# Optimization experiments

Hardware: AMD Instinct MI355X
Metric: run time of the kernel (lower is better)

Reference implementation:

```python
import jax, jax.numpy as jnp
import numpy as np

N = 50000      # nodes
E = 800000     # edges
D_IN = 512
D_OUT = 512
EDGE_DIM = 3


def setup_inputs() -> dict:
    key = jax.random.key(0)
    k = jax.random.split(key, 6)
    x = jax.random.normal(k[0], (N, D_IN), dtype=jnp.float32)
    edge_index = jax.random.randint(k[1], (2, E), 0, N, dtype=jnp.int64)
    edge_attr = jax.random.normal(k[2], (E, EDGE_DIM), dtype=jnp.float32)
    # xavier-uniform-ish init for linear weights
    lim1 = (6.0 / (D_IN + D_OUT)) ** 0.5
    lin_w = jax.random.uniform(k[3], (D_OUT, D_IN), minval=-lim1, maxval=lim1, dtype=jnp.float32)
    lin_b = jnp.zeros((D_OUT,), dtype=jnp.float32)
    lim2 = (6.0 / (EDGE_DIM + 1)) ** 0.5
    conf_w = jax.random.uniform(k[4], (1, EDGE_DIM), minval=-lim2, maxval=lim2, dtype=jnp.float32)
    conf_b = jnp.zeros((1,), dtype=jnp.float32)
    return {"x": x, "edge_index": edge_index, "edge_attr": edge_attr,
            "lin_w": lin_w, "lin_b": lin_b, "conf_w": conf_w, "conf_b": conf_b}


def reference(x, edge_index, edge_attr, lin_w, lin_b, conf_w, conf_b):
    row, col = edge_index[0], edge_index[1]
    # edge confidence weight: sigmoid(conf_lin(edge_attr)) -> [E]
    edge_weight = jax.nn.sigmoid(edge_attr @ conf_w.T + conf_b)[:, 0]
    # degree of source nodes (count of row occurrences), inverse sqrt with inf/nan -> 0
    deg = jnp.zeros((x.shape[0],), dtype=x.dtype).at[row].add(1.0)
    deg_safe = jnp.where(deg > 0, deg, 1.0)
    deg_inv_sqrt = jnp.where(deg > 0, jax.lax.rsqrt(deg_safe), 0.0)
    norm = deg_inv_sqrt[row] * deg_inv_sqrt[col] * edge_weight  # [E]
    norm = jnp.where(jnp.isnan(norm), 0.0, norm)
    # gather-scale-scatter: out[col] += x[row] * norm
    out = jnp.zeros_like(x).at[col].add(x[row] * norm[:, None])
    return out @ lin_w.T + lin_b
```

## Files before the change

kernel.cpp:

```cpp
#include <hip/hip_runtime.h>

#define NDIM 512
#define CAP  64

typedef __bf16 bf16x8 __attribute__((ext_vector_type(8)));
typedef float  f32x4  __attribute__((ext_vector_type(4)));

__device__ inline ushort f2bf(float f) {
    uint b = __float_as_uint(f);
    return (ushort)((b + 0x7fffu + ((b >> 16) & 1u)) >> 16);
}
__device__ inline float bflo(uint u) { return __uint_as_float(u << 16); }
__device__ inline float bfhi(uint u) { return __uint_as_float(u & 0xffff0000u); }
__device__ inline uint packbf(float lo, float hi) {
    return ((uint)f2bf(hi) << 16) | (uint)f2bf(lo);
}

__device__ inline void gload16(const ushort* g, ushort* l) {
    __builtin_amdgcn_global_load_lds(
        (const __attribute__((address_space(1))) uint*)g,
        (__attribute__((address_space(3))) uint*)l, 16, 0, 0);
}

__global__ __launch_bounds__(256) void prep_kernel(
        const float* __restrict__ x,  ushort* __restrict__ xh,
        const float* __restrict__ w,  ushort* __restrict__ wh,
        const int* __restrict__ ei, int* __restrict__ deg_row,
        int nx4, int nw4, int E, int gX, int gW) {
    int b = blockIdx.x;
    if (b < gX) {
        int i = b * 256 + threadIdx.x;
        if (i < nx4) {
            float4 v = ((const float4*)x)[i];
            ushort4 o;
            o.x = f2bf(v.x); o.y = f2bf(v.y); o.z = f2bf(v.z); o.w = f2bf(v.w);
            ((ushort4*)xh)[i] = o;
        }
    } else if (b < gX + gW) {
        int i = (b - gX) * 256 + threadIdx.x;
        if (i < nw4) {
            float4 v = ((const float4*)w)[i];
            ushort4 o;
            o.x = f2bf(v.x); o.y = f2bf(v.y); o.z = f2bf(v.z); o.w = f2bf(v.w);
            ((ushort4*)wh)[i] = o;
        }
    } else {
        int e = (b - gX - gW) * 256 + threadIdx.x;
        if (e < E) atomicAdd(&deg_row[ei[e]], 1);
    }
}

__global__ __launch_bounds__(256) void fill_kernel(
        const int* __restrict__ ei, const float* __restrict__ ea,
        const int* __restrict__ deg,
        const float* __restrict__ conf_w, const float* __restrict__ conf_b,
        int* __restrict__ fill_cnt, int2* __restrict__ rn, int E) {
    int e = blockIdx.x * 256 + threadIdx.x;
    if (e >= E) return;
    int row = ei[e];
    int col = ei[E + e];
    float w = ea[(size_t)e*3+0]*conf_w[0] + ea[(size_t)e*3+1]*conf_w[1]
            + ea[(size_t)e*3+2]*conf_w[2] + conf_b[0];
    w = 1.0f / (1.0f + __expf(-w));
    int dr = deg[row], dc = deg[col];
    float ir = (dr > 0) ? rsqrtf((float)dr) : 0.0f;
    float ic = (dc > 0) ? rsqrtf((float)dc) : 0.0f;
    float nm = ir * ic * w;
    int pos = (col << 6) + atomicAdd(&fill_cnt[col], 1);
    rn[pos] = make_int2(row, __float_as_int(nm));
}

#define ACC8(u, nm)                                                     \
    a0 = fmaf(bflo((u).x), (nm), a0); a1 = fmaf(bfhi((u).x), (nm), a1); \
    a2 = fmaf(bflo((u).y), (nm), a2); a3 = fmaf(bfhi((u).y), (nm), a3); \
    a4 = fmaf(bflo((u).z), (nm), a4); a5 = fmaf(bfhi((u).z), (nm), a5); \
    a6 = fmaf(bflo((u).w), (nm), a6); a7 = fmaf(bfhi((u).w), (nm), a7);

__global__ __launch_bounds__(256) void agg_kernel(
        const ushort* __restrict__ xh, const int2* __restrict__ rn,
        const int* __restrict__ cnt, ushort* __restrict__ aggh, int N) {
    int wid  = threadIdx.x >> 6;
    int lane = threadIdx.x & 63;
    int node = blockIdx.x * 4 + wid;
    if (node >= N) return;
    int start = node << 6;
    int end   = start + ((cnt[node] + 7) & ~7);
    const ushort* xc = xh + lane * 8;
    float a0 = 0.f, a1 = 0.f, a2 = 0.f, a3 = 0.f;
    float a4 = 0.f, a5 = 0.f, a6 = 0.f, a7 = 0.f;
    int p = start;
    if (p < end) {
        int4 q0 = *(const int4*)(rn + p + 0);
        int4 q1 = *(const int4*)(rn + p + 2);
        int4 q2 = *(const int4*)(rn + p + 4);
        int4 q3 = *(const int4*)(rn + p + 6);
        for (;;) {
            uint4 u0 = *(const uint4*)(xc + ((size_t)(uint)q0.x << 9));
            uint4 u1 = *(const uint4*)(xc + ((size_t)(uint)q0.z << 9));
            uint4 u2 = *(const uint4*)(xc + ((size_t)(uint)q1.x << 9));
            uint4 u3 = *(const uint4*)(xc + ((size_t)(uint)q1.z << 9));
            uint4 u4 = *(const uint4*)(xc + ((size_t)(uint)q2.x << 9));
            uint4 u5 = *(const uint4*)(xc + ((size_t)(uint)q2.z << 9));
            uint4 u6 = *(const uint4*)(xc + ((size_t)(uint)q3.x << 9));
            uint4 u7 = *(const uint4*)(xc + ((size_t)(uint)q3.z << 9));
            float n0 = __int_as_float(q0.y), n1 = __int_as_float(q0.w);
            float n2 = __int_as_float(q1.y), n3 = __int_as_float(q1.w);
            float n4 = __int_as_float(q2.y), n5 = __int_as_float(q2.w);
            float n6 = __int_as_float(q3.y), n7 = __int_as_float(q3.w);
            p += 8;
            bool more = p < end;
            int q = more ? p : start;
            q0 = *(const int4*)(rn + q + 0);
            q1 = *(const int4*)(rn + q + 2);
            q2 = *(const int4*)(rn + q + 4);
            q3 = *(const int4*)(rn + q + 6);
            ACC8(u0, n0); ACC8(u1, n1); ACC8(u2, n2); ACC8(u3, n3);
            ACC8(u4, n4); ACC8(u5, n5); ACC8(u6, n6); ACC8(u7, n7);
            if (!more) break;
        }
    }
    uint4 o;
    o.x = packbf(a0, a1);
    o.y = packbf(a2, a3);
    o.z = packbf(a4, a5);
    o.w = packbf(a6, a7);
    *(uint4*)(aggh + (size_t)node * NDIM + lane * 8) = o;
}

__global__ __launch_bounds__(256) void mfma_gemm(
        const ushort* __restrict__ A,
        const ushort* __restrict__ B,
        const float* __restrict__ bias,
        float* __restrict__ out, int M) {
    __shared__ ushort As[128 * 32];
    __shared__ ushort Bs[128 * 32];
    int Mb = (M + 127) >> 7;
    int lin = blockIdx.x;
    int full = (Mb >> 3) << 5;
    int mb, nb;
    if (lin < full) {
        mb = ((lin >> 5) << 3) + (lin & 7);
        nb = (lin >> 3) & 3;
    } else {
        int r = lin - full;
        int mrem = Mb & 7;
        mb = ((Mb >> 3) << 3) + (r % mrem);
        nb = r / mrem;
    }
    int m0 = mb << 7;
    int n0 = nb << 7;
    int tid  = threadIdx.x;
    int lane = tid & 63;
    int wave = tid >> 6;
    int wr = wave >> 1, wc = wave & 1;
    int quad = lane >> 4, l16 = lane & 15;
    int lrow = lane >> 2, lcol = (lane & 3) << 3;

    f32x4 acc[4][4] = {};

    for (int k0 = 0; k0 < NDIM; k0 += 32) {
#pragma unroll
        for (int i = 0; i < 2; ++i) {
            int ch = wave * 2 + i;
            int r  = ch * 16 + lrow;
            int gm = m0 + r; if (gm >= M) gm = M - 1;
            gload16(A + ((size_t)gm << 9) + k0 + lcol, &As[ch * 512]);
            gload16(B + ((size_t)(n0 + r) << 9) + k0 + lcol, &Bs[ch * 512]);
        }
        __syncthreads();
#pragma unroll
        for (int mt = 0; mt < 4; ++mt) {
            bf16x8 a = *(const bf16x8*)&As[(wr * 64 + mt * 16 + l16) * 32 + quad * 8];
#pragma unroll
            for (int nt = 0; nt < 4; ++nt) {
                bf16x8 b = *(const bf16x8*)&Bs[(wc * 64 + nt * 16 + l16) * 32 + quad * 8];
                acc[mt][nt] = __builtin_amdgcn_mfma_f32_16x16x32_bf16(a, b, acc[mt][nt], 0, 0, 0);
            }
        }
        __syncthreads();
    }
#pragma unroll
    for (int mt = 0; mt < 4; ++mt) {
#pragma unroll
        for (int nt = 0; nt < 4; ++nt) {
            int gn = n0 + wc * 64 + nt * 16 + l16;
            float bv = bias[gn];
#pragma unroll
            for (int r = 0; r < 4; ++r) {
                int gm = m0 + wr * 64 + mt * 16 + quad * 4 + r;
                if (gm < M) out[(size_t)gm * NDIM + gn] = acc[mt][nt][r] + bv;
            }
        }
    }
}

extern "C" void kernel_launch(void* const* d_in, const int* in_sizes, int n_in,
                              void* d_out, int out_size, void* d_ws, size_t ws_size,
                              hipStream_t stream) {
    const float* x      = (const float*)d_in[0];
    const int*   ei     = (const int*)  d_in[1];
    const float* ea     = (const float*)d_in[2];
    const float* lin_w  = (const float*)d_in[3];
    const float* lin_b  = (const float*)d_in[4];
    const float* conf_w = (const float*)d_in[5];
    const float* conf_b = (const float*)d_in[6];
    float* out = (float*)d_out;

    int N = in_sizes[0] / NDIM;
    int E = in_sizes[2] / 3;

    char* p = (char*)d_ws;
    auto alloc = [&](size_t bytes) {
        char* q = p;
        p += (bytes + 255) & ~(size_t)255;
        return q;
    };
    ushort* aggh       = (ushort*)alloc((size_t)N * NDIM * sizeof(ushort));
    ushort* wh         = (ushort*)alloc((size_t)NDIM * NDIM * sizeof(ushort));
    int*   deg_row     = (int*)  alloc((size_t)N * sizeof(int));
    int*   fill_cnt    = (int*)  alloc((size_t)N * sizeof(int));

    ushort* xh = (ushort*)d_out;
    int2*   rn = (int2*)((char*)d_out + (size_t)N * NDIM * sizeof(ushort));

    size_t zero_cnt_bytes = (size_t)((char*)(fill_cnt + N) - (char*)deg_row);
    (void)hipMemsetAsync(deg_row, 0, zero_cnt_bytes, stream);
    (void)hipMemsetAsync(rn, 0, (size_t)N * CAP * sizeof(int2), stream);

    int gE = (E + 255) / 256;
    int x4 = (N * NDIM) / 4, w4 = (NDIM * NDIM) / 4;
    int gX = (x4 + 255) / 256, gW = (w4 + 255) / 256;
    prep_kernel  <<<gX + gW + gE, 256, 0, stream>>>(x, xh, lin_w, wh, ei,
                                                    deg_row, x4, w4, E, gX, gW);
    fill_kernel  <<<gE, 256, 0, stream>>>(ei, ea, deg_row, conf_w, conf_b,
                                          fill_cnt, rn, E);
    agg_kernel   <<<(N + 3) / 4, 256, 0, stream>>>(xh, rn, fill_cnt, aggh, N);
    int Mb = (N + 127) >> 7;
    mfma_gemm    <<<Mb * 4, 256, 0, stream>>>(aggh, wh, lin_b, out, N);
}
```

Before: 436.3 us.

## Fuse CSR fill into prep kernel and defer degree normalization to aggregation

Merges the edge fill step into the prep kernel by storing only the sigmoid edge weight in the bucket, so fill no longer waits on the degree pass. The aggregation kernel now looks up source degrees per edge and applies the column rsqrt once at the end. It also drops the memset of the bucket array by masking padded slots in-kernel. This removes one kernel launch, a sequential dependency and a large memset, but adds per-edge degree gathers and rsqrt work inside the aggregation loop.

```diff
diff --git a/kernel.cpp b/kernel.cpp
--- a/kernel.cpp
+++ b/kernel.cpp
@@ -25,8 +25,11 @@
 __global__ __launch_bounds__(256) void prep_kernel(
         const float* __restrict__ x,  ushort* __restrict__ xh,
         const float* __restrict__ w,  ushort* __restrict__ wh,
-        const int* __restrict__ ei, int* __restrict__ deg_row,
-        int nx4, int nw4, int E, int gX, int gW) {
+        const int* __restrict__ ei,   const float* __restrict__ ea,
+        const float* __restrict__ conf_w, const float* __restrict__ conf_b,
+        int* __restrict__ deg_row, int* __restrict__ fill_cnt,
+        int2* __restrict__ rn,
+        int nx4, int nw4, int E, int gX, int gW, int gE) {
     int b = blockIdx.x;
     if (b < gX) {
         int i = b * 256 + threadIdx.x;
@@ -44,30 +47,21 @@
             o.x = f2bf(v.x); o.y = f2bf(v.y); o.z = f2bf(v.z); o.w = f2bf(v.w);
             ((ushort4*)wh)[i] = o;
         }
-    } else {
+    } else if (b < gX + gW + gE) {
         int e = (b - gX - gW) * 256 + threadIdx.x;
         if (e < E) atomicAdd(&deg_row[ei[e]], 1);
-    }
-}
-
-__global__ __launch_bounds__(256) void fill_kernel(
-        const int* __restrict__ ei, const float* __restrict__ ea,
-        const int* __restrict__ deg,
-        const float* __restrict__ conf_w, const float* __restrict__ conf_b,
-        int* __restrict__ fill_cnt, int2* __restrict__ rn, int E) {
-    int e = blockIdx.x * 256 + threadIdx.x;
-    if (e >= E) return;
-    int row = ei[e];
-    int col = ei[E + e];
-    float w = ea[(size_t)e*3+0]*conf_w[0] + ea[(size_t)e*3+1]*conf_w[1]
-            + ea[(size_t)e*3+2]*conf_w[2] + conf_b[0];
-    w = 1.0f / (1.0f + __expf(-w));
-    int dr = deg[row], dc = deg[col];
-    float ir = (dr > 0) ? rsqrtf((float)dr) : 0.0f;
-    float ic = (dc > 0) ? rsqrtf((float)dc) : 0.0f;
-    float nm = ir * ic * w;
-    int pos = (col << 6) + atomicAdd(&fill_cnt[col], 1);
-    rn[pos] = make_int2(row, __float_as_int(nm));
+    } else {
+        int e = (b - gX - gW - gE) * 256 + threadIdx.x;
+        if (e < E) {
+            int row = ei[e];
+            int col = ei[E + e];
+            float wv = ea[(size_t)e*3+0]*conf_w[0] + ea[(size_t)e*3+1]*conf_w[1]
+                     + ea[(size_t)e*3+2]*conf_w[2] + conf_b[0];
+            wv = 1.0f / (1.0f + __expf(-wv));
+            int pos = (col << 6) + atomicAdd(&fill_cnt[col], 1);
+            rn[pos] = make_int2(row, __float_as_int(wv));
+        }
+    }
 }
 
 #define ACC8(u, nm)                                                     \
@@ -76,24 +70,45 @@
     a4 = fmaf(bflo((u).z), (nm), a4); a5 = fmaf(bfhi((u).z), (nm), a5); \
     a6 = fmaf(bflo((u).w), (nm), a6); a7 = fmaf(bfhi((u).w), (nm), a7);
 
+#define LOADQ(P)                                                           \
+    q0 = *(const int4*)(rn + (P) + 0);                                     \
+    q1 = *(const int4*)(rn + (P) + 2);                                     \
+    q2 = *(const int4*)(rn + (P) + 4);                                     \
+    q3 = *(const int4*)(rn + (P) + 6);                                     \
+    q0.x = ((P)+0 < limit) ? q0.x : 0;  q0.y = ((P)+0 < limit) ? q0.y : 0; \
+    q0.z = ((P)+1 < limit) ? q0.z : 0;  q0.w = ((P)+1 < limit) ? q0.w : 0; \
+    q1.x = ((P)+2 < limit) ? q1.x : 0;  q1.y = ((P)+2 < limit) ? q1.y : 0; \
+    q1.z = ((P)+3 < limit) ? q1.z : 0;  q1.w = ((P)+3 < limit) ? q1.w : 0; \
+    q2.x = ((P)+4 < limit) ? q2.x : 0;  q2.y = ((P)+4 < limit) ? q2.y : 0; \
+    q2.z = ((P)+5 < limit) ? q2.z : 0;  q2.w = ((P)+5 < limit) ? q2.w : 0; \
+    q3.x = ((P)+6 < limit) ? q3.x : 0;  q3.y = ((P)+6 < limit) ? q3.y : 0; \
+    q3.z = ((P)+7 < limit) ? q3.z : 0;  q3.w = ((P)+7 < limit) ? q3.w : 0; \
+    d0 = deg[(uint)q0.x]; d1 = deg[(uint)q0.z];                            \
+    d2 = deg[(uint)q1.x]; d3 = deg[(uint)q1.z];                            \
+    d4 = deg[(uint)q2.x]; d5 = deg[(uint)q2.z];                            \
+    d6 = deg[(uint)q3.x]; d7 = deg[(uint)q3.z];
+
 __global__ __launch_bounds__(256) void agg_kernel(
         const ushort* __restrict__ xh, const int2* __restrict__ rn,
-        const int* __restrict__ cnt, ushort* __restrict__ aggh, int N) {
+        const int* __restrict__ cnt_arr, const int* __restrict__ deg,
+        ushort* __restrict__ aggh, int N) {
     int wid  = threadIdx.x >> 6;
     int lane = threadIdx.x & 63;
     int node = blockIdx.x * 4 + wid;
     if (node >= N) return;
-    int start = node << 6;
-    int end   = start + ((cnt[node] + 7) & ~7);
+    int cnt = cnt_arr[node];
+    int dc  = deg[node];
+    float discol = (dc > 0) ? rsqrtf((float)dc) : 0.0f;
     const ushort* xc = xh + lane * 8;
     float a0 = 0.f, a1 = 0.f, a2 = 0.f, a3 = 0.f;
     float a4 = 0.f, a5 = 0.f, a6 = 0.f, a7 = 0.f;
-    int p = start;
-    if (p < end) {
-        int4 q0 = *(const int4*)(rn + p + 0);
-        int4 q1 = *(const int4*)(rn + p + 2);
-        int4 q2 = *(const int4*)(rn + p + 4);
-        int4 q3 = *(const int4*)(rn + p + 6);
+    int start = node << 6;
+    int limit = start + cnt;
+    if (cnt > 0) {
+        int4 q0, q1, q2, q3;
+        int d0, d1, d2, d3, d4, d5, d6, d7;
+        int p = start;
+        LOADQ(p);
         for (;;) {
             uint4 u0 = *(const uint4*)(xc + ((size_t)(uint)q0.x << 9));
             uint4 u1 = *(const uint4*)(xc + ((size_t)(uint)q0.z << 9));
@@ -103,22 +118,31 @@
             uint4 u5 = *(const uint4*)(xc + ((size_t)(uint)q2.z << 9));
             uint4 u6 = *(const uint4*)(xc + ((size_t)(uint)q3.x << 9));
             uint4 u7 = *(const uint4*)(xc + ((size_t)(uint)q3.z << 9));
-            float n0 = __int_as_float(q0.y), n1 = __int_as_float(q0.w);
-            float n2 = __int_as_float(q1.y), n3 = __int_as_float(q1.w);
-            float n4 = __int_as_float(q2.y), n5 = __int_as_float(q2.w);
-            float n6 = __int_as_float(q3.y), n7 = __int_as_float(q3.w);
+            float w0 = __int_as_float(q0.y), w1 = __int_as_float(q0.w);
+            float w2 = __int_as_float(q1.y), w3 = __int_as_float(q1.w);
+            float w4 = __int_as_float(q2.y), w5 = __int_as_float(q2.w);
+            float w6 = __int_as_float(q3.y), w7 = __int_as_float(q3.w);
+            int c0 = d0, c1 = d1, c2 = d2, c3 = d3;
+            int c4 = d4, c5 = d5, c6 = d6, c7 = d7;
             p += 8;
-            bool more = p < end;
-            int q = more ? p : start;
-            q0 = *(const int4*)(rn + q + 0);
-            q1 = *(const int4*)(rn + q + 2);
-            q2 = *(const int4*)(rn + q + 4);
-            q3 = *(const int4*)(rn + q + 6);
-            ACC8(u0, n0); ACC8(u1, n1); ACC8(u2, n2); ACC8(u3, n3);
-            ACC8(u4, n4); ACC8(u5, n5); ACC8(u6, n6); ACC8(u7, n7);
+            bool more = p < limit;
+            int np = more ? p : start;
+            LOADQ(np);
+            float nm0 = (c0 > 0 ? rsqrtf((float)c0) : 0.f) * w0;
+            float nm1 = (c1 > 0 ? rsqrtf((float)c1) : 0.f) * w1;
+            float nm2 = (c2 > 0 ? rsqrtf((float)c2) : 0.f) * w2;
+            float nm3 = (c3 > 0 ? rsqrtf((float)c3) : 0.f) * w3;
+            float nm4 = (c4 > 0 ? rsqrtf((float)c4) : 0.f) * w4;
+            float nm5 = (c5 > 0 ? rsqrtf((float)c5) : 0.f) * w5;
+            float nm6 = (c6 > 0 ? rsqrtf((float)c6) : 0.f) * w6;
+            float nm7 = (c7 > 0 ? rsqrtf((float)c7) : 0.f) * w7;
+            ACC8(u0, nm0); ACC8(u1, nm1); ACC8(u2, nm2); ACC8(u3, nm3);
+            ACC8(u4, nm4); ACC8(u5, nm5); ACC8(u6, nm6); ACC8(u7, nm7);
             if (!more) break;
         }
     }
+    a0 *= discol; a1 *= discol; a2 *= discol; a3 *= discol;
+    a4 *= discol; a5 *= discol; a6 *= discol; a7 *= discol;
     uint4 o;
     o.x = packbf(a0, a1);
     o.y = packbf(a2, a3);
@@ -225,16 +249,14 @@
 
     size_t zero_cnt_bytes = (size_t)((char*)(fill_cnt + N) - (char*)deg_row);
     (void)hipMemsetAsync(deg_row, 0, zero_cnt_bytes, stream);
-    (void)hipMemsetAsync(rn, 0, (size_t)N * CAP * sizeof(int2), stream);
 
     int gE = (E + 255) / 256;
     int x4 = (N * NDIM) / 4, w4 = (NDIM * NDIM) / 4;
     int gX = (x4 + 255) / 256, gW = (w4 + 255) / 256;
-    prep_kernel  <<<gX + gW + gE, 256, 0, stream>>>(x, xh, lin_w, wh, ei,
-                                                    deg_row, x4, w4, E, gX, gW);
-    fill_kernel  <<<gE, 256, 0, stream>>>(ei, ea, deg_row, conf_w, conf_b,
-                                          fill_cnt, rn, E);
-    agg_kernel   <<<(N + 3) / 4, 256, 0, stream>>>(xh, rn, fill_cnt, aggh, N);
+    prep_kernel  <<<gX + gW + 2 * gE, 256, 0, stream>>>(
+        x, xh, lin_w, wh, ei, ea, conf_w, conf_b,
+        deg_row, fill_cnt, rn, x4, w4, E, gX, gW, gE);
+    agg_kernel   <<<(N + 3) / 4, 256, 0, stream>>>(xh, rn, fill_cnt, deg_row, aggh, N);
     int Mb = (N + 127) >> 7;
     mfma_gemm    <<<Mb * 4, 256, 0, stream>>>(aggh, wh, lin_b, out, N);
 }
```

Result: no change. 434.2 us (-0.5%).
